# Kernel optimization log

Measured on AMD Instinct MI355X. Metric: run time of the kernel, lower is better.

Reference implementation:

```python
import jax, jax.numpy as jnp
import numpy as np

D_MODEL = 1280
D_BOTTLE = 64
LN_EPS = 1e-5


def setup_inputs() -> dict:
    key = jax.random.key(0)
    k1, k2, k3, k4, k5 = jax.random.split(key, 5)
    x = jax.random.normal(k1, (16, 1500, D_MODEL), dtype=jnp.float32)
    # LayerNorm params (torch default: weight=1, bias=0; use random-ish gamma for a stronger test)
    gamma = jnp.ones((D_MODEL,), dtype=jnp.float32)
    beta = jnp.zeros((D_MODEL,), dtype=jnp.float32)
    # Linear weights stored torch-style: [out, in]
    w_down = jax.random.normal(k2, (D_BOTTLE, D_MODEL), dtype=jnp.float32) * (1.0 / np.sqrt(D_MODEL))
    b_down = jax.random.normal(k3, (D_BOTTLE,), dtype=jnp.float32) * 0.01
    # up_proj is zero-initialized in the module; use small random values so gradients/outputs are nontrivial
    w_up = jax.random.normal(k4, (D_MODEL, D_BOTTLE), dtype=jnp.float32) * 0.01
    b_up = jax.random.normal(k5, (D_MODEL,), dtype=jnp.float32) * 0.01
    return {"x": x, "gamma": gamma, "beta": beta, "w_down": w_down, "b_down": b_down, "w_up": w_up, "b_up": b_up}


def reference(x, gamma, beta, w_down, b_down, w_up, b_up):
    # LayerNorm over last dim
    mean = jnp.mean(x, axis=-1, keepdims=True)
    var = jnp.mean(jnp.square(x - mean), axis=-1, keepdims=True)
    h = (x - mean) * jax.lax.rsqrt(var + LN_EPS) * gamma + beta
    # down-proj -> GELU -> up-proj (torch GELU default = exact erf form)
    h = jnp.einsum('bsd,kd->bsk', h, w_down) + b_down   # [B,S,64]
    h = jax.nn.gelu(h, approximate=False)
    h = jnp.einsum('bsk,dk->bsd', h, w_up) + b_up       # [B,S,1280]
    return h + x
```

## Files before the change

### kernel.cpp

```cpp
#include <hip/hip_runtime.h>
#include <hip/hip_bf16.h>

#define D_MODEL  1280
#define D_BOTTLE 64
#define LN_EPS   1e-5f
#define TM       8
#define ROWB     2560
#define GP       72

typedef __attribute__((ext_vector_type(8))) short short8;
typedef __attribute__((ext_vector_type(4))) float floatx4;

static __device__ inline unsigned short f2bf(float f) {
    __hip_bfloat16 h = __float2bfloat16(f);
    return *reinterpret_cast<unsigned short*>(&h);
}
static __device__ inline float bf2f(unsigned short u) {
    unsigned int v = ((unsigned int)u) << 16;
    return __uint_as_float(v);
}

__global__ void prep_weights(const float* __restrict__ wd, const float* __restrict__ gamma,
                             const float* __restrict__ wu,
                             unsigned short* __restrict__ wg, unsigned short* __restrict__ wu_b) {
    int i = blockIdx.x * blockDim.x + threadIdx.x;
    if (i < D_MODEL * D_BOTTLE) {
        int k = i % D_MODEL;
        wg[i]   = f2bf(wd[i] * gamma[k]);
        wu_b[i] = f2bf(wu[i]);
    }
}

__global__ void prep_reduce(const unsigned short* __restrict__ wg, const float* __restrict__ wd,
                            const float* __restrict__ beta, const float* __restrict__ b_down,
                            float* __restrict__ colsum, float* __restrict__ bd2) {
    const int n = blockIdx.x;
    const int t = threadIdx.x;
    float cs = 0.f, bb = 0.f;
    for (int k = t; k < D_MODEL; k += 256) {
        cs += bf2f(wg[n * D_MODEL + k]);
        bb += wd[n * D_MODEL + k] * beta[k];
    }
    #pragma unroll
    for (int m = 1; m < 64; m <<= 1) {
        cs += __shfl_xor(cs, m);
        bb += __shfl_xor(bb, m);
    }
    __shared__ float scs[4], sbb[4];
    if ((t & 63) == 0) { scs[t >> 6] = cs; sbb[t >> 6] = bb; }
    __syncthreads();
    if (t == 0) {
        colsum[n] = scs[0] + scs[1] + scs[2] + scs[3];
        bd2[n]    = b_down[n] + sbb[0] + sbb[1] + sbb[2] + sbb[3];
    }
}

__global__ __launch_bounds__(256, 6) void adapter_kernel(
    const float* __restrict__ x,
    const unsigned short* __restrict__ wg, const float* __restrict__ colsum,
    const float* __restrict__ bd2,
    const unsigned short* __restrict__ wu_b, const float* __restrict__ b_up,
    float* __restrict__ out)
{
    __shared__ unsigned char  h_raw[TM * ROWB];
    __shared__ unsigned short g_lds[TM * GP];
    __shared__ float s_mean[TM], s_rinv[TM];

    const int tid  = threadIdx.x;
    const int wave = tid >> 6;
    const int lane = tid & 63;
    const int r0   = blockIdx.x * TM;

    {
        const int rloc = tid >> 5;
        const int li   = tid & 31;
        const float* xrow = x + (size_t)(r0 + rloc) * D_MODEL;
        float4 v0 = *reinterpret_cast<const float4*>(xrow + li * 4 +    0);
        float4 v1 = *reinterpret_cast<const float4*>(xrow + li * 4 +  128);
        float4 v2 = *reinterpret_cast<const float4*>(xrow + li * 4 +  256);
        float4 v3 = *reinterpret_cast<const float4*>(xrow + li * 4 +  384);
        float4 v4 = *reinterpret_cast<const float4*>(xrow + li * 4 +  512);
        float4 v5 = *reinterpret_cast<const float4*>(xrow + li * 4 +  640);
        float4 v6 = *reinterpret_cast<const float4*>(xrow + li * 4 +  768);
        float4 v7 = *reinterpret_cast<const float4*>(xrow + li * 4 +  896);
        float4 v8 = *reinterpret_cast<const float4*>(xrow + li * 4 + 1024);
        float4 v9 = *reinterpret_cast<const float4*>(xrow + li * 4 + 1152);

        float s = 0.f, sq = 0.f;
        #define ACC4(v) { s += v.x + v.y + v.z + v.w; sq += v.x*v.x + v.y*v.y + v.z*v.z + v.w*v.w; }
        ACC4(v0) ACC4(v1) ACC4(v2) ACC4(v3) ACC4(v4)
        ACC4(v5) ACC4(v6) ACC4(v7) ACC4(v8) ACC4(v9)
        #undef ACC4
        #pragma unroll
        for (int m = 1; m < 32; m <<= 1) {
            s  += __shfl_xor(s, m);
            sq += __shfl_xor(sq, m);
        }
        const float mean = s * (1.f / D_MODEL);
        const float var  = sq * (1.f / D_MODEL) - mean * mean;
        if (li == 0) { s_mean[rloc] = mean; s_rinv[rloc] = rsqrtf(var + LN_EPS); }

        const int swz = rloc << 4;
        #define ST4(v, t) { ushort4 pk; pk.x = f2bf(v.x); pk.y = f2bf(v.y); pk.z = f2bf(v.z); pk.w = f2bf(v.w); \
            *reinterpret_cast<ushort4*>(h_raw + rloc * ROWB + ((li * 8 + 256 * (t)) ^ swz)) = pk; }
        ST4(v0,0) ST4(v1,1) ST4(v2,2) ST4(v3,3) ST4(v4,4)
        ST4(v5,5) ST4(v6,6) ST4(v7,7) ST4(v8,8) ST4(v9,9)
        #undef ST4
    }
    __syncthreads();

    const int l15   = lane & 15;
    const int khalf = lane >> 4;
    const int lr    = l15 & 7;
    const int nn    = wave * 16 + l15;

    floatx4 acc = {0.f, 0.f, 0.f, 0.f};
    {
        const unsigned short* brow = wg + (size_t)nn * D_MODEL + khalf * 8;
        const unsigned char*  abase = h_raw + lr * ROWB;
        const int aswz = lr << 4;
        #pragma unroll 4
        for (int kk = 0; kk < 40; ++kk) {
            short8 a = *reinterpret_cast<const short8*>(abase + ((kk * 64 + khalf * 16) ^ aswz));
            short8 b = *reinterpret_cast<const short8*>(brow + kk * 32);
            acc = __builtin_amdgcn_mfma_f32_16x16x32_bf16(a, b, acc, 0, 0, 0);
        }
    }

    {
        const float cs  = colsum[nn];
        const float bdn = bd2[nn];
        if (khalf < 2) {
            #pragma unroll
            for (int r = 0; r < 4; ++r) {
                const int m = khalf * 4 + r;
                const float yv = s_rinv[m] * (acc[r] - s_mean[m] * cs) + bdn;
                const float gv = 0.5f * yv * (1.f + erff(yv * 0.70710678118654752f));
                g_lds[m * GP + nn] = f2bf(gv);
            }
        }
    }
    __syncthreads();

    short8 ga0 = *reinterpret_cast<const short8*>(g_lds + lr * GP +  0 + khalf * 8);
    short8 ga1 = *reinterpret_cast<const short8*>(g_lds + lr * GP + 32 + khalf * 8);

    #pragma unroll 2
    for (int i = 0; i < 20; ++i) {
        const int d = (i * 4 + wave) * 16 + l15;
        const unsigned short* bptr = wu_b + (size_t)d * D_BOTTLE + khalf * 8;
        short8 b0 = *reinterpret_cast<const short8*>(bptr);
        short8 b1 = *reinterpret_cast<const short8*>(bptr + 32);
        floatx4 acc2 = {0.f, 0.f, 0.f, 0.f};
        acc2 = __builtin_amdgcn_mfma_f32_16x16x32_bf16(ga0, b0, acc2, 0, 0, 0);
        acc2 = __builtin_amdgcn_mfma_f32_16x16x32_bf16(ga1, b1, acc2, 0, 0, 0);
        const float bu = b_up[d];
        if (khalf < 2) {
            #pragma unroll
            for (int r = 0; r < 4; ++r) {
                const int m = khalf * 4 + r;
                const unsigned short xr16 =
                    *reinterpret_cast<const unsigned short*>(h_raw + m * ROWB + ((d * 2) ^ (m << 4)));
                out[(size_t)(r0 + m) * D_MODEL + d] = acc2[r] + bu + bf2f(xr16);
            }
        }
    }
}

extern "C" void kernel_launch(void* const* d_in, const int* in_sizes, int n_in,
                              void* d_out, int out_size, void* d_ws, size_t ws_size,
                              hipStream_t stream) {
    const float* x      = (const float*)d_in[0];
    const float* gamma  = (const float*)d_in[1];
    const float* beta   = (const float*)d_in[2];
    const float* w_down = (const float*)d_in[3];
    const float* b_down = (const float*)d_in[4];
    const float* w_up   = (const float*)d_in[5];
    const float* b_up   = (const float*)d_in[6];
    float* out = (float*)d_out;

    unsigned short* wg   = (unsigned short*)d_ws;
    unsigned short* wu_b = wg + D_MODEL * D_BOTTLE;
    float* colsum = (float*)(wu_b + D_MODEL * D_BOTTLE);
    float* bd2    = colsum + D_BOTTLE;

    prep_weights<<<(D_MODEL * D_BOTTLE + 255) / 256, 256, 0, stream>>>(w_down, gamma, w_up, wg, wu_b);
    prep_reduce<<<D_BOTTLE, 256, 0, stream>>>(wg, w_down, beta, b_down, colsum, bd2);

    const int rows = in_sizes[0] / D_MODEL;
    adapter_kernel<<<rows / TM, 256, 0, stream>>>(x, wg, colsum, bd2, wu_b, b_up, out);
}
```

Measured before the change: 317.5 us.

## Stage x tile in LDS as fp32 via direct global-to-LDS loads

Replaces the register load of x followed by a bf16 swizzled LDS store with buffer global_load_lds DMA that writes fp32 rows straight into padded shared memory. LayerNorm statistics are then computed from LDS, the bf16 conversion moves into the MFMA loop, and the residual now uses the exact fp32 x. LDS use per block doubles, so launch bounds drop from 6 to 3 blocks per CU, which lowers occupancy on a memory-bound kernel. The residual add also becomes more accurate.

```diff
diff --git a/kernel.cpp b/kernel.cpp
--- a/kernel.cpp
+++ b/kernel.cpp
@@ -5,7 +5,7 @@
 #define D_BOTTLE 64
 #define LN_EPS   1e-5f
 #define TM       8
-#define ROWB     2560
+#define XS       1284
 #define GP       72
 
 typedef __attribute__((ext_vector_type(8))) short short8;
@@ -18,6 +18,14 @@
 static __device__ inline float bf2f(unsigned short u) {
     unsigned int v = ((unsigned int)u) << 16;
     return __uint_as_float(v);
+}
+static __device__ inline short8 cvt8(float4 a0, float4 a1) {
+    short8 r;
+    r[0] = (short)f2bf(a0.x); r[1] = (short)f2bf(a0.y);
+    r[2] = (short)f2bf(a0.z); r[3] = (short)f2bf(a0.w);
+    r[4] = (short)f2bf(a1.x); r[5] = (short)f2bf(a1.y);
+    r[6] = (short)f2bf(a1.z); r[7] = (short)f2bf(a1.w);
+    return r;
 }
 
 __global__ void prep_weights(const float* __restrict__ wd, const float* __restrict__ gamma,
@@ -55,14 +63,14 @@
     }
 }
 
-__global__ __launch_bounds__(256, 6) void adapter_kernel(
+__global__ __launch_bounds__(256, 3) void adapter_kernel(
     const float* __restrict__ x,
     const unsigned short* __restrict__ wg, const float* __restrict__ colsum,
     const float* __restrict__ bd2,
     const unsigned short* __restrict__ wu_b, const float* __restrict__ b_up,
     float* __restrict__ out)
 {
-    __shared__ unsigned char  h_raw[TM * ROWB];
+    __shared__ float xs[TM * XS];
     __shared__ unsigned short g_lds[TM * GP];
     __shared__ float s_mean[TM], s_rinv[TM];
 
@@ -72,25 +80,33 @@
     const int r0   = blockIdx.x * TM;
 
     {
-        const int rloc = tid >> 5;
-        const int li   = tid & 31;
-        const float* xrow = x + (size_t)(r0 + rloc) * D_MODEL;
-        float4 v0 = *reinterpret_cast<const float4*>(xrow + li * 4 +    0);
-        float4 v1 = *reinterpret_cast<const float4*>(xrow + li * 4 +  128);
-        float4 v2 = *reinterpret_cast<const float4*>(xrow + li * 4 +  256);
-        float4 v3 = *reinterpret_cast<const float4*>(xrow + li * 4 +  384);
-        float4 v4 = *reinterpret_cast<const float4*>(xrow + li * 4 +  512);
-        float4 v5 = *reinterpret_cast<const float4*>(xrow + li * 4 +  640);
-        float4 v6 = *reinterpret_cast<const float4*>(xrow + li * 4 +  768);
-        float4 v7 = *reinterpret_cast<const float4*>(xrow + li * 4 +  896);
-        float4 v8 = *reinterpret_cast<const float4*>(xrow + li * 4 + 1024);
-        float4 v9 = *reinterpret_cast<const float4*>(xrow + li * 4 + 1152);
+        #pragma unroll
+        for (int rr = 0; rr < 2; ++rr) {
+            const int row = wave * 2 + rr;
+            const float* gsrc = x + (size_t)(r0 + row) * D_MODEL + lane * 4;
+            float* ldst = &xs[row * XS];
+            #pragma unroll
+            for (int c = 0; c < 5; ++c) {
+                __builtin_amdgcn_global_load_lds(
+                    (const __attribute__((address_space(1))) unsigned int*)(gsrc + c * 256),
+                    (__attribute__((address_space(3))) unsigned int*)(ldst + c * 256),
+                    16, 0, 0);
+            }
+        }
+    }
+    __syncthreads();
 
+    {
+        const int srow = tid >> 5;
+        const int sli  = tid & 31;
+        const float* xr = &xs[srow * XS + sli * 4];
         float s = 0.f, sq = 0.f;
-        #define ACC4(v) { s += v.x + v.y + v.z + v.w; sq += v.x*v.x + v.y*v.y + v.z*v.z + v.w*v.w; }
-        ACC4(v0) ACC4(v1) ACC4(v2) ACC4(v3) ACC4(v4)
-        ACC4(v5) ACC4(v6) ACC4(v7) ACC4(v8) ACC4(v9)
-        #undef ACC4
+        #pragma unroll
+        for (int t = 0; t < 10; ++t) {
+            float4 v = *reinterpret_cast<const float4*>(xr + t * 128);
+            s  += v.x + v.y + v.z + v.w;
+            sq += v.x * v.x + v.y * v.y + v.z * v.z + v.w * v.w;
+        }
         #pragma unroll
         for (int m = 1; m < 32; m <<= 1) {
             s  += __shfl_xor(s, m);
@@ -98,14 +114,7 @@
         }
         const float mean = s * (1.f / D_MODEL);
         const float var  = sq * (1.f / D_MODEL) - mean * mean;
-        if (li == 0) { s_mean[rloc] = mean; s_rinv[rloc] = rsqrtf(var + LN_EPS); }
-
-        const int swz = rloc << 4;
-        #define ST4(v, t) { ushort4 pk; pk.x = f2bf(v.x); pk.y = f2bf(v.y); pk.z = f2bf(v.z); pk.w = f2bf(v.w); \
-            *reinterpret_cast<ushort4*>(h_raw + rloc * ROWB + ((li * 8 + 256 * (t)) ^ swz)) = pk; }
-        ST4(v0,0) ST4(v1,1) ST4(v2,2) ST4(v3,3) ST4(v4,4)
-        ST4(v5,5) ST4(v6,6) ST4(v7,7) ST4(v8,8) ST4(v9,9)
-        #undef ST4
+        if (sli == 0) { s_mean[srow] = mean; s_rinv[srow] = rsqrtf(var + LN_EPS); }
     }
     __syncthreads();
 
@@ -117,13 +126,13 @@
     floatx4 acc = {0.f, 0.f, 0.f, 0.f};
     {
         const unsigned short* brow = wg + (size_t)nn * D_MODEL + khalf * 8;
-        const unsigned char*  abase = h_raw + lr * ROWB;
-        const int aswz = lr << 4;
+        const float* arow = &xs[lr * XS + khalf * 8];
         #pragma unroll 4
         for (int kk = 0; kk < 40; ++kk) {
-            short8 a = *reinterpret_cast<const short8*>(abase + ((kk * 64 + khalf * 16) ^ aswz));
-            short8 b = *reinterpret_cast<const short8*>(brow + kk * 32);
-            acc = __builtin_amdgcn_mfma_f32_16x16x32_bf16(a, b, acc, 0, 0, 0);
+            float4 a0 = *reinterpret_cast<const float4*>(arow + kk * 32);
+            float4 a1 = *reinterpret_cast<const float4*>(arow + kk * 32 + 4);
+            short8 b  = *reinterpret_cast<const short8*>(brow + kk * 32);
+            acc = __builtin_amdgcn_mfma_f32_16x16x32_bf16(cvt8(a0, a1), b, acc, 0, 0, 0);
         }
     }
 
@@ -159,9 +168,7 @@
             #pragma unroll
             for (int r = 0; r < 4; ++r) {
                 const int m = khalf * 4 + r;
-                const unsigned short xr16 =
-                    *reinterpret_cast<const unsigned short*>(h_raw + m * ROWB + ((d * 2) ^ (m << 4)));
-                out[(size_t)(r0 + m) * D_MODEL + d] = acc2[r] + bu + bf2f(xr16);
+                out[(size_t)(r0 + m) * D_MODEL + d] = acc2[r] + bu + xs[m * XS + d];
             }
         }
     }
```

Result: no change. 321.6 us (+1.3%).
